# Performance work log

Measured on AMD Instinct MI355X. Metric: run time of the kernel, lower is better.

The kernel has to match this reference:

```python
import jax, jax.numpy as jnp
import numpy as np

STRIDE, PAD, DIL, GROUPS, DG = 1, 1, 1, 1, 1
KH = KW = 3


def setup_inputs() -> dict:
    key = jax.random.key(0)
    k1, k2, k3, k4 = jax.random.split(key, 4)
    N, Cin, Cout, H, W = 8, 256, 256, 64, 64
    Ho = (H + 2 * PAD - (DIL * (KH - 1) + 1)) // STRIDE + 1
    Wo = (W + 2 * PAD - (DIL * (KW - 1) + 1)) // STRIDE + 1
    x = jax.random.normal(k1, (N, Cin, H, W), jnp.float32)
    offset = jax.random.normal(k2, (N, 2 * DG * KH * KW, Ho, Wo), jnp.float32)
    mask = jax.random.uniform(k3, (N, DG * KH * KW, Ho, Wo), jnp.float32)
    fan_in = (Cin // GROUPS) * KH * KW
    weight = jax.random.normal(k4, (Cout, Cin // GROUPS, KH, KW), jnp.float32) * np.float32(np.sqrt(2.0 / fan_in))
    bias = jnp.zeros((Cout,), jnp.float32)
    return {"x": x, "offset": offset, "mask": mask, "weight": weight, "bias": bias}


def _dcn_forward(x, offset, mask, weight, bias):
    # Modulated deformable conv v2 (DCNv2), NCHW layout.
    N, Cin, H, W = x.shape
    Cout, Cg, kh, kw = weight.shape
    K = kh * kw
    Ho, Wo = offset.shape[2], offset.shape[3]
    Cp = Cin // DG  # channels per deformable group

    # offset channels laid out as [DG, K, (dy, dx)]
    off = offset.reshape(N, DG, K, 2, Ho, Wo)
    ky = (jnp.arange(K) // kw) * DIL
    kx = (jnp.arange(K) % kw) * DIL
    base_y = (jnp.arange(Ho) * STRIDE - PAD)[None, :, None] + ky[:, None, None]  # [K,Ho,1]
    base_x = (jnp.arange(Wo) * STRIDE - PAD)[None, None, :] + kx[:, None, None]  # [K,1,Wo]
    y = base_y[None, None] + off[:, :, :, 0]   # [N,DG,K,Ho,Wo] sampling rows
    xs = base_x[None, None] + off[:, :, :, 1]  # [N,DG,K,Ho,Wo] sampling cols

    xg = x.reshape(N, DG, Cp, H * W)  # flat spatial for gathers
    y0 = jnp.floor(y)
    x0 = jnp.floor(xs)
    val = jnp.zeros((N, DG, Cp, K, Ho, Wo), x.dtype)
    # bilinear interpolation with zero padding outside the image
    for iy in (0.0, 1.0):
        for ix in (0.0, 1.0):
            yc = y0 + iy
            xc = x0 + ix
            wgt = (1.0 - jnp.abs(y - yc)) * (1.0 - jnp.abs(xs - xc))
            valid = (yc >= 0) & (yc < H) & (xc >= 0) & (xc < W)
            wgt = jnp.where(valid, wgt, 0.0)
            yci = jnp.clip(yc, 0, H - 1).astype(jnp.int32)
            xci = jnp.clip(xc, 0, W - 1).astype(jnp.int32)
            idx = (yci * W + xci).reshape(N, DG, 1, K * Ho * Wo)
            g = jnp.take_along_axis(xg, idx, axis=3).reshape(N, DG, Cp, K, Ho, Wo)
            val = val + g * wgt[:, :, None]

    # modulation mask, broadcast over channels of each deformable group
    col = val * mask.reshape(N, DG, 1, K, Ho, Wo)
    col = col.reshape(N, GROUPS, Cin // GROUPS, K, Ho, Wo)
    wr = weight.reshape(GROUPS, Cout // GROUPS, Cg, K)
    out = jnp.einsum('gock,ngckhw->ngohw', wr, col).reshape(N, Cout, Ho, Wo)
    return out + bias[None, :, None, None]


def reference(x, offset, mask, weight, bias):
    return _dcn_forward(x, offset, mask, weight, bias)
```

## Files before the change

kernel.cpp:

```cpp
#include <hip/hip_runtime.h>
#include <hip/hip_bf16.h>
#include <stdint.h>


#define XH 64
#define XW 64
#define CIN 256
#define COUT 256
#define NK 9

typedef __attribute__((ext_vector_type(8))) short short8;
typedef __attribute__((ext_vector_type(4))) float floatx4;
typedef __attribute__((ext_vector_type(2))) float floatx2;
typedef __attribute__((ext_vector_type(4))) int   intx4;

__device__ __forceinline__ short f32_to_bf16_rne(float f) {
    union { float f; uint32_t u; } v; v.f = f;
    uint32_t u = v.u;
    uint32_t r = (u + 0x7FFFu + ((u >> 16) & 1u)) >> 16;
    return (short)(uint16_t)r;
}
__device__ __forceinline__ float bf16_to_f32(short s) {
    union { uint32_t u; float f; } v;
    v.u = ((uint32_t)(uint16_t)s) << 16;
    return v.f;
}
__device__ __forceinline__ floatx2 bf16x2_to_f32x2(uint32_t u) {
    union { uint32_t u; float f; } lo, hi;
    lo.u = u << 16;
    hi.u = u & 0xFFFF0000u;
    floatx2 r; r.x = lo.f; r.y = hi.f;
    return r;
}

__global__ void dcn_prep(const float* __restrict__ x, const float* __restrict__ w,
                         short* __restrict__ xT, short* __restrict__ w3) {
    int b = blockIdx.x;
    int tid = threadIdx.x;
    if (b < 512) {
        int xcd = b & 7, slot = b >> 3;
        int h = xcd * 8 + (slot & 7);
        int n = slot >> 3;
        int q = tid & 15;
        int cgh = tid >> 4;
        short8* ob = (short8*)(xT + ((size_t)(n * XH + h)) * (XW * CIN));
        for (int it = 0; it < 2; ++it) {
            int cg = cgh + it * 16;
            const float* xb = x + ((size_t)(n * CIN + cg * 8)) * (XH * XW)
                                + h * XW + q * 4;
            floatx4 r[8];
#pragma unroll
            for (int j = 0; j < 8; ++j)
                r[j] = *(const floatx4*)(xb + (size_t)j * (XH * XW));
#pragma unroll
            for (int jw = 0; jw < 4; ++jw) {
                short8 pk;
#pragma unroll
                for (int j = 0; j < 8; ++j) pk[j] = f32_to_bf16_rne(r[j][jw]);
                ob[(q * 4 + jw) * 32 + cg] = pk;
            }
        }
    } else {
        int gidx = (b - 512) * 256 + tid;
        int lane = gidx & 63;
        int mt   = (gidx >> 6) & 15;
        int t    = gidx >> 10;
        int ks   = t & 7;
        int k    = t >> 3;
        int co = mt * 16 + (lane & 15);
        int c0 = ks * 32 + (lane >> 4) * 8;
        short8 pk;
#pragma unroll
        for (int j = 0; j < 8; ++j)
            pk[j] = f32_to_bf16_rne(w[(co * CIN + c0 + j) * NK + k]);
        *(short8*)&w3[(size_t)gidx * 8] = pk;
    }
}

__launch_bounds__(512, 4)
__global__ void dcn_fused3(const short* __restrict__ xT,
                           const float* __restrict__ off,
                           const float* __restrict__ msk,
                           const short* __restrict__ w3,
                           const float* __restrict__ bias,
                           float* __restrict__ out) {
    __shared__ short   colF[2048 * 8];
    __shared__ floatx4 pairW[576];
    __shared__ intx4   pairO[576];

    const int bid = blockIdx.x;
    const int xcd = bid & 7, slot = bid >> 3;
    const int ho = xcd * 8 + (slot & 7);
    const int n  = slot >> 3;
    const int tid  = threadIdx.x;
    const int wave = tid >> 6;
    const int lane = tid & 63;

    for (int p = tid; p < 576; p += 512) {
        int wo = p & 63, k = p >> 6;
        int obase = ((n * 18 + 2 * k) * XH + ho) * XW + wo;
        float dy = off[obase];
        float dx = off[obase + XH * XW];
        float mm = msk[((n * NK + k) * XH + ho) * XW + wo];
        float y  = (float)(ho - 1 + k / 3) + dy;
        float xs = (float)(wo - 1 + k % 3) + dx;
        float y0f = floorf(y), x0f = floorf(xs);
        float fy = y - y0f, fx = xs - x0f;
        int y0 = (int)y0f, x0 = (int)x0f;
        float vy0 = (y0 >= 0  && y0 < XH)     ? 1.f : 0.f;
        float vy1 = (y0 >= -1 && y0 < XH - 1) ? 1.f : 0.f;
        float vx0 = (x0 >= 0  && x0 < XW)     ? 1.f : 0.f;
        float vx1 = (x0 >= -1 && x0 < XW - 1) ? 1.f : 0.f;
        floatx4 wv;
        wv.x = (1.f - fy) * (1.f - fx) * mm * vy0 * vx0;
        wv.y = (1.f - fy) * fx         * mm * vy0 * vx1;
        wv.z = fy         * (1.f - fx) * mm * vy1 * vx0;
        wv.w = fy         * fx         * mm * vy1 * vx1;
        int y0c = min(max(y0, 0), XH - 1), y1c = min(max(y0 + 1, 0), XH - 1);
        int x0c = min(max(x0, 0), XW - 1), x1c = min(max(x0 + 1, 0), XW - 1);
        intx4 ov;
        ov.x = y0c * XW + x0c; ov.y = y0c * XW + x1c;
        ov.z = y1c * XW + x0c; ov.w = y1c * XW + x1c;
        pairW[p] = wv;
        pairO[p] = ov;
    }
    __syncthreads();

    floatx4 acc[2][4];
#pragma unroll
    for (int mt = 0; mt < 2; ++mt)
#pragma unroll
        for (int nt = 0; nt < 4; ++nt)
            acc[mt][nt] = (floatx4)(0.f);

    const short8* xTv = (const short8*)(xT + (size_t)n * (XH * XW * CIN));
    const short8* w3v = (const short8*)w3;
    const int quad = lane >> 4, cl = lane & 15;

    union U8 { short8 s; uint32_t u[4]; };

    for (int k = 0; k < NK; ++k) {
        if (k) __syncthreads();
        for (int it = 0; it < 4; ++it) {
            int idx = it * 512 + tid;
            int chg = idx & 31;
            int pos = idx >> 5;
            int p = k * 64 + pos;
            floatx4 wv = pairW[p];
            intx4   ov = pairO[p];
            U8 s00, s01, s10, s11, pk;
            s00.s = xTv[(size_t)ov.x * 32 + chg];
            s01.s = xTv[(size_t)ov.y * 32 + chg];
            s10.s = xTv[(size_t)ov.z * 32 + chg];
            s11.s = xTv[(size_t)ov.w * 32 + chg];
#pragma unroll
            for (int i = 0; i < 4; ++i) {
                floatx2 v = bf16x2_to_f32x2(s00.u[i]) * wv.x
                          + bf16x2_to_f32x2(s01.u[i]) * wv.y
                          + bf16x2_to_f32x2(s10.u[i]) * wv.z
                          + bf16x2_to_f32x2(s11.u[i]) * wv.w;
                float2 ff; ff.x = v.x; ff.y = v.y;
                __hip_bfloat162 hb = __float22bfloat162_rn(ff);
                __builtin_memcpy(&pk.u[i], &hb, 4);
            }
            int g = chg * 64 + (pos ^ (chg & 7));
            *(short8*)&colF[g * 8] = pk.s;
        }
        __syncthreads();

        for (int ks = 0; ks < 8; ++ks) {
            short8 afrag[2];
#pragma unroll
            for (int mt = 0; mt < 2; ++mt)
                afrag[mt] = w3v[(((k * 8 + ks) * 16) + (wave * 2 + mt)) * 64 + lane];
            short8 bfrag[4];
            int cr = ks * 4 + quad;
            int gb = cr * 64, sw = cr & 7;
#pragma unroll
            for (int nt = 0; nt < 4; ++nt)
                bfrag[nt] = *(const short8*)&colF[(gb + ((nt * 16 + cl) ^ sw)) * 8];
#pragma unroll
            for (int mt = 0; mt < 2; ++mt)
#pragma unroll
                for (int nt = 0; nt < 4; ++nt)
                    acc[mt][nt] = __builtin_amdgcn_mfma_f32_16x16x32_bf16(
                        afrag[mt], bfrag[nt], acc[mt][nt], 0, 0, 0);
        }
    }

#pragma unroll
    for (int mt = 0; mt < 2; ++mt) {
        int cobase = (wave * 2 + mt) * 16 + quad * 4;
#pragma unroll
        for (int r = 0; r < 4; ++r) {
            int co = cobase + r;
            float b = bias[co];
            float* op = out + (((size_t)n * COUT + co) * XH + ho) * XW;
#pragma unroll
            for (int nt = 0; nt < 4; ++nt)
                op[nt * 16 + cl] = acc[mt][nt][r] + b;
        }
    }
}

__global__ void dcn_wprep_v1(const float* __restrict__ w, short* __restrict__ w3) {
    int idx = blockIdx.x * 256 + threadIdx.x;
    if (idx >= 8 * 9 * 16 * 64 * 8) return;
    int j    = idx & 7;
    int lane = (idx >> 3) & 63;
    int mt   = (idx >> 9) & 15;
    int t    = idx >> 13;
    int ks   = t % 9;
    int cc   = t / 9;
    int co = mt * 16 + (lane & 15);
    int c  = cc * 32 + (lane >> 4) * 8 + j;
    w3[idx] = f32_to_bf16_rne(w[(co * CIN + c) * NK + ks]);
}

__launch_bounds__(256, 2)
__global__ void dcn_fused_v1(const float* __restrict__ x,
                             const float* __restrict__ off,
                             const float* __restrict__ msk,
                             const short* __restrict__ w3,
                             const float* __restrict__ bias,
                             float* __restrict__ out) {
    __shared__ short  colF[2304 * 8];
    __shared__ floatx4 pairW[576];
    __shared__ intx4   pairO[576];

    const int bid = blockIdx.x;
    const int n  = bid >> 6;
    const int ho = bid & 63;
    const int tid  = threadIdx.x;
    const int wave = tid >> 6;
    const int lane = tid & 63;

    for (int p = tid; p < 576; p += 256) {
        int wo = p & 63, k = p >> 6;
        int obase = ((n * 18 + 2 * k) * XH + ho) * XW + wo;
        float dy = off[obase];
        float dx = off[obase + XH * XW];
        float mm = msk[((n * NK + k) * XH + ho) * XW + wo];
        float y  = (float)(ho - 1 + k / 3) + dy;
        float xs = (float)(wo - 1 + k % 3) + dx;
        float y0f = floorf(y), x0f = floorf(xs);
        float fy = y - y0f, fx = xs - x0f;
        int y0 = (int)y0f, x0 = (int)x0f;
        float vy0 = (y0 >= 0  && y0 < XH)     ? 1.f : 0.f;
        float vy1 = (y0 >= -1 && y0 < XH - 1) ? 1.f : 0.f;
        float vx0 = (x0 >= 0  && x0 < XW)     ? 1.f : 0.f;
        float vx1 = (x0 >= -1 && x0 < XW - 1) ? 1.f : 0.f;
        floatx4 wv;
        wv.x = (1.f - fy) * (1.f - fx) * mm * vy0 * vx0;
        wv.y = (1.f - fy) * fx         * mm * vy0 * vx1;
        wv.z = fy         * (1.f - fx) * mm * vy1 * vx0;
        wv.w = fy         * fx         * mm * vy1 * vx1;
        int y0c = min(max(y0, 0), XH - 1), y1c = min(max(y0 + 1, 0), XH - 1);
        int x0c = min(max(x0, 0), XW - 1), x1c = min(max(x0 + 1, 0), XW - 1);
        intx4 ov;
        ov.x = y0c * XW + x0c; ov.y = y0c * XW + x1c;
        ov.z = y1c * XW + x0c; ov.w = y1c * XW + x1c;
        pairW[p] = wv;
        pairO[p] = ov;
    }
    __syncthreads();

    floatx4 acc[4][4];
#pragma unroll
    for (int mt = 0; mt < 4; ++mt)
#pragma unroll
        for (int nt = 0; nt < 4; ++nt)
            acc[mt][nt] = (floatx4)(0.f);

    const float* xn = x + (size_t)n * CIN * (XH * XW);
    const short8* w3v = (const short8*)w3;

    for (int cc = 0; cc < 8; ++cc) {
        __syncthreads();
        for (int it = 0; it < 9; ++it) {
            int item = it * 256 + tid;
            int pos  = item & 63;
            int r    = item >> 6;
            int k    = r >> 2;
            int csub = r & 3;
            int p = k * 64 + pos;
            floatx4 wv = pairW[p];
            intx4   ov = pairO[p];
            const float* xc = xn + (size_t)(cc * 32 + csub * 8) * (XH * XW);
            short8 pk;
#pragma unroll
            for (int i = 0; i < 8; ++i) {
                const float* xp = xc + i * (XH * XW);
                float v = wv.x * xp[ov.x] + wv.y * xp[ov.y] +
                          wv.z * xp[ov.z] + wv.w * xp[ov.w];
                pk[i] = f32_to_bf16_rne(v);
            }
            *(short8*)&colF[(((k * 4 + csub) * 64) + pos) * 8] = pk;
        }
        __syncthreads();

        const int quad = lane >> 4, cl = lane & 15;
        for (int ks = 0; ks < 9; ++ks) {
            short8 afrag[4];
#pragma unroll
            for (int mt = 0; mt < 4; ++mt) {
                int mtg = wave * 4 + mt;
                afrag[mt] = w3v[(((cc * 9 + ks) * 16 + mtg) * 64) + lane];
            }
            short8 bfrag[4];
#pragma unroll
            for (int nt = 0; nt < 4; ++nt)
                bfrag[nt] = *(const short8*)
                    &colF[(((ks * 4 + quad) * 64) + nt * 16 + cl) * 8];
#pragma unroll
            for (int mt = 0; mt < 4; ++mt)
#pragma unroll
                for (int nt = 0; nt < 4; ++nt)
                    acc[mt][nt] = __builtin_amdgcn_mfma_f32_16x16x32_bf16(
                        afrag[mt], bfrag[nt], acc[mt][nt], 0, 0, 0);
        }
    }

    const int quad = lane >> 4, cl = lane & 15;
#pragma unroll
    for (int mt = 0; mt < 4; ++mt) {
        int cobase = (wave * 4 + mt) * 16 + quad * 4;
#pragma unroll
        for (int r = 0; r < 4; ++r) {
            int co = cobase + r;
            float b = bias[co];
            float* op = out + (((size_t)n * COUT + co) * XH + ho) * XW;
#pragma unroll
            for (int nt = 0; nt < 4; ++nt)
                op[nt * 16 + cl] = acc[mt][nt][r] + b;
        }
    }
}

__global__ void dcn_naive(const float* __restrict__ x,
                          const float* __restrict__ off,
                          const float* __restrict__ msk,
                          const float* __restrict__ w,
                          const float* __restrict__ bias,
                          float* __restrict__ out) {
    int idx = blockIdx.x * 256 + threadIdx.x;
    if (idx >= 8 * COUT * XH * XW) return;
    int wo = idx & 63, ho = (idx >> 6) & 63, co = (idx >> 12) & 255, n = idx >> 20;
    float acc = bias[co];
    for (int k = 0; k < NK; ++k) {
        int obase = ((n * 18 + 2 * k) * XH + ho) * XW + wo;
        float dy = off[obase];
        float dx = off[obase + XH * XW];
        float mm = msk[((n * NK + k) * XH + ho) * XW + wo];
        float y  = (float)(ho - 1 + k / 3) + dy;
        float xs = (float)(wo - 1 + k % 3) + dx;
        float y0f = floorf(y), x0f = floorf(xs);
        float fy = y - y0f, fx = xs - x0f;
        int y0 = (int)y0f, x0 = (int)x0f;
        float vy0 = (y0 >= 0  && y0 < XH)     ? 1.f : 0.f;
        float vy1 = (y0 >= -1 && y0 < XH - 1) ? 1.f : 0.f;
        float vx0 = (x0 >= 0  && x0 < XW)     ? 1.f : 0.f;
        float vx1 = (x0 >= -1 && x0 < XW - 1) ? 1.f : 0.f;
        float w00 = (1.f - fy) * (1.f - fx) * mm * vy0 * vx0;
        float w01 = (1.f - fy) * fx         * mm * vy0 * vx1;
        float w10 = fy         * (1.f - fx) * mm * vy1 * vx0;
        float w11 = fy         * fx         * mm * vy1 * vx1;
        int y0c = min(max(y0, 0), XH - 1), y1c = min(max(y0 + 1, 0), XH - 1);
        int x0c = min(max(x0, 0), XW - 1), x1c = min(max(x0 + 1, 0), XW - 1);
        int o00 = y0c * XW + x0c, o01 = y0c * XW + x1c;
        int o10 = y1c * XW + x0c, o11 = y1c * XW + x1c;
        for (int c = 0; c < CIN; ++c) {
            const float* xp = x + ((size_t)(n * CIN + c)) * (XH * XW);
            float v = w00 * xp[o00] + w01 * xp[o01] + w10 * xp[o10] + w11 * xp[o11];
            acc += v * w[(co * CIN + c) * NK + k];
        }
    }
    out[idx] = acc;
}

extern "C" void kernel_launch(void* const* d_in, const int* in_sizes, int n_in,
                              void* d_out, int out_size, void* d_ws, size_t ws_size,
                              hipStream_t stream) {
    const float* x    = (const float*)d_in[0];
    const float* off  = (const float*)d_in[1];
    const float* msk  = (const float*)d_in[2];
    const float* w    = (const float*)d_in[3];
    const float* bias = (const float*)d_in[4];
    float* out = (float*)d_out;

    const size_t W3_BYTES = (size_t)9 * 8 * 16 * 64 * 8 * sizeof(short);
    const size_t XT_BYTES = (size_t)8 * XH * XW * CIN * sizeof(short);

    if (ws_size >= W3_BYTES + XT_BYTES) {
        short* w3 = (short*)d_ws;
        short* xT = (short*)((char*)d_ws + W3_BYTES);
        dcn_prep<<<512 + 288, 256, 0, stream>>>(x, w, xT, w3);
        dcn_fused3<<<8 * 64, 512, 0, stream>>>(xT, off, msk, w3, bias, out);
    } else if (ws_size >= W3_BYTES) {
        short* w3 = (short*)d_ws;
        dcn_wprep_v1<<<(8 * 9 * 16 * 64 * 8 + 255) / 256, 256, 0, stream>>>(w, w3);
        dcn_fused_v1<<<8 * 64, 256, 0, stream>>>(x, off, msk, w3, bias, out);
    } else {
        dcn_naive<<<(8 * COUT * XH * XW + 255) / 256, 256, 0, stream>>>(
            x, off, msk, w, bias, out);
    }
}
```

Baseline: 151.8 us.

## Double-buffer column tile and overlap bilinear gathers with MFMA in half-K steps

The column tile in LDS is split into two half-size buffers, and the reduction is processed in 18 half-channel steps. Each step issues the global gathers for the next step, runs MFMAs on the current buffer, then does the bilinear blend into the other buffer. This needs only one barrier per step instead of two per kernel tap. Gather offsets are also prescaled by 32 to save address math. The cost is more registers held live across the MFMA loop, which at 512 threads with launch bounds of 4 may cause spills or lower occupancy.

```diff
diff --git a/kernel.cpp b/kernel.cpp
--- a/kernel.cpp
+++ b/kernel.cpp
@@ -31,6 +31,25 @@
     hi.u = u & 0xFFFF0000u;
     floatx2 r; r.x = lo.f; r.y = hi.f;
     return r;
+}
+
+union U8 { short8 s; uint32_t u[4]; };
+
+__device__ __forceinline__ short8 bilerp8(const U8& a, const U8& b,
+                                          const U8& c, const U8& d,
+                                          floatx4 wv) {
+    U8 pk;
+#pragma unroll
+    for (int i = 0; i < 4; ++i) {
+        floatx2 v = bf16x2_to_f32x2(a.u[i]) * wv.x
+                  + bf16x2_to_f32x2(b.u[i]) * wv.y
+                  + bf16x2_to_f32x2(c.u[i]) * wv.z
+                  + bf16x2_to_f32x2(d.u[i]) * wv.w;
+        float2 ff; ff.x = v.x; ff.y = v.y;
+        __hip_bfloat162 hb = __float22bfloat162_rn(ff);
+        __builtin_memcpy(&pk.u[i], &hb, 4);
+    }
+    return pk.s;
 }
 
 __global__ void dcn_prep(const float* __restrict__ x, const float* __restrict__ w,
@@ -78,13 +97,13 @@
 }
 
 __launch_bounds__(512, 4)
-__global__ void dcn_fused3(const short* __restrict__ xT,
+__global__ void dcn_fused4(const short* __restrict__ xT,
                            const float* __restrict__ off,
                            const float* __restrict__ msk,
                            const short* __restrict__ w3,
                            const float* __restrict__ bias,
                            float* __restrict__ out) {
-    __shared__ short   colF[2048 * 8];
+    __shared__ short   colF[2][1024 * 8];
     __shared__ floatx4 pairW[576];
     __shared__ intx4   pairO[576];
 
@@ -95,6 +114,7 @@
     const int tid  = threadIdx.x;
     const int wave = tid >> 6;
     const int lane = tid & 63;
+    const int quad = lane >> 4, cl = lane & 15;
 
     for (int p = tid; p < 576; p += 512) {
         int wo = p & 63, k = p >> 6;
@@ -119,8 +139,8 @@
         int y0c = min(max(y0, 0), XH - 1), y1c = min(max(y0 + 1, 0), XH - 1);
         int x0c = min(max(x0, 0), XW - 1), x1c = min(max(x0 + 1, 0), XW - 1);
         intx4 ov;
-        ov.x = y0c * XW + x0c; ov.y = y0c * XW + x1c;
-        ov.z = y1c * XW + x0c; ov.w = y1c * XW + x1c;
+        ov.x = (y0c * XW + x0c) * 32; ov.y = (y0c * XW + x1c) * 32;
+        ov.z = (y1c * XW + x0c) * 32; ov.w = (y1c * XW + x1c) * 32;
         pairW[p] = wv;
         pairO[p] = ov;
     }
@@ -135,57 +155,83 @@
 
     const short8* xTv = (const short8*)(xT + (size_t)n * (XH * XW * CIN));
     const short8* w3v = (const short8*)w3;
-    const int quad = lane >> 4, cl = lane & 15;
-
-    union U8 { short8 s; uint32_t u[4]; };
-
-    for (int k = 0; k < NK; ++k) {
-        if (k) __syncthreads();
-        for (int it = 0; it < 4; ++it) {
+
+    {
+        U8 s[2][4]; floatx4 wv2[2]; int gd[2];
+#pragma unroll
+        for (int it = 0; it < 2; ++it) {
             int idx = it * 512 + tid;
-            int chg = idx & 31;
-            int pos = idx >> 5;
-            int p = k * 64 + pos;
-            floatx4 wv = pairW[p];
-            intx4   ov = pairO[p];
-            U8 s00, s01, s10, s11, pk;
-            s00.s = xTv[(size_t)ov.x * 32 + chg];
-            s01.s = xTv[(size_t)ov.y * 32 + chg];
-            s10.s = xTv[(size_t)ov.z * 32 + chg];
-            s11.s = xTv[(size_t)ov.w * 32 + chg];
-#pragma unroll
-            for (int i = 0; i < 4; ++i) {
-                floatx2 v = bf16x2_to_f32x2(s00.u[i]) * wv.x
-                          + bf16x2_to_f32x2(s01.u[i]) * wv.y
-                          + bf16x2_to_f32x2(s10.u[i]) * wv.z
-                          + bf16x2_to_f32x2(s11.u[i]) * wv.w;
-                float2 ff; ff.x = v.x; ff.y = v.y;
-                __hip_bfloat162 hb = __float22bfloat162_rn(ff);
-                __builtin_memcpy(&pk.u[i], &hb, 4);
+            int chg = idx & 15;
+            int pos = idx >> 4;
+            wv2[it] = pairW[pos];
+            intx4 ov = pairO[pos];
+            s[it][0].s = xTv[ov.x + chg];
+            s[it][1].s = xTv[ov.y + chg];
+            s[it][2].s = xTv[ov.z + chg];
+            s[it][3].s = xTv[ov.w + chg];
+            gd[it] = chg * 64 + (pos ^ (chg & 7));
+        }
+#pragma unroll
+        for (int it = 0; it < 2; ++it)
+            *(short8*)&colF[0][gd[it] * 8] =
+                bilerp8(s[it][0], s[it][1], s[it][2], s[it][3], wv2[it]);
+    }
+    __syncthreads();
+
+    auto step = [&](int ht, const short* rb, short* wb) {
+        const int k = ht >> 1, h = ht & 1;
+        const bool pre = (ht < 17);
+        U8 s[2][4]; floatx4 wv2[2]; int gd[2];
+        if (pre) {
+            const int nht = ht + 1, nk = nht >> 1, nh = nht & 1;
+#pragma unroll
+            for (int it = 0; it < 2; ++it) {
+                int idx = it * 512 + tid;
+                int chg_l = idx & 15;
+                int pos = idx >> 4;
+                int p = nk * 64 + pos;
+                wv2[it] = pairW[p];
+                intx4 ov = pairO[p];
+                int chg = nh * 16 + chg_l;
+                s[it][0].s = xTv[ov.x + chg];
+                s[it][1].s = xTv[ov.y + chg];
+                s[it][2].s = xTv[ov.z + chg];
+                s[it][3].s = xTv[ov.w + chg];
+                gd[it] = chg_l * 64 + (pos ^ (chg_l & 7));
             }
-            int g = chg * 64 + (pos ^ (chg & 7));
-            *(short8*)&colF[g * 8] = pk.s;
-        }
-        __syncthreads();
-
-        for (int ks = 0; ks < 8; ++ks) {
-            short8 afrag[2];
+        }
+        const short8* cb = (const short8*)rb;
+        const int kb = (k * 8 + h * 4) * 16 + wave * 2;
+#pragma unroll
+        for (int ks = 0; ks < 4; ++ks) {
+            const int cr = ks * 4 + quad, sw = cr & 7, gb = cr * 64;
+            short8 afr[2], bfr[4];
 #pragma unroll
             for (int mt = 0; mt < 2; ++mt)
-                afrag[mt] = w3v[(((k * 8 + ks) * 16) + (wave * 2 + mt)) * 64 + lane];
-            short8 bfrag[4];
-            int cr = ks * 4 + quad;
-            int gb = cr * 64, sw = cr & 7;
+                afr[mt] = w3v[(kb + ks * 16 + mt) * 64 + lane];
 #pragma unroll
             for (int nt = 0; nt < 4; ++nt)
-                bfrag[nt] = *(const short8*)&colF[(gb + ((nt * 16 + cl) ^ sw)) * 8];
+                bfr[nt] = cb[gb + ((nt * 16 + cl) ^ sw)];
 #pragma unroll
             for (int mt = 0; mt < 2; ++mt)
 #pragma unroll
                 for (int nt = 0; nt < 4; ++nt)
                     acc[mt][nt] = __builtin_amdgcn_mfma_f32_16x16x32_bf16(
-                        afrag[mt], bfrag[nt], acc[mt][nt], 0, 0, 0);
-        }
+                        afr[mt], bfr[nt], acc[mt][nt], 0, 0, 0);
+        }
+        if (pre) {
+#pragma unroll
+            for (int it = 0; it < 2; ++it)
+                *(short8*)&wb[gd[it] * 8] =
+                    bilerp8(s[it][0], s[it][1], s[it][2], s[it][3], wv2[it]);
+            __syncthreads();
+        }
+    };
+
+#pragma unroll 1
+    for (int hp = 0; hp < 9; ++hp) {
+        step(2 * hp,     colF[0], colF[1]);
+        step(2 * hp + 1, colF[1], colF[0]);
     }
 
 #pragma unroll
@@ -395,7 +441,7 @@
         short* w3 = (short*)d_ws;
         short* xT = (short*)((char*)d_ws + W3_BYTES);
         dcn_prep<<<512 + 288, 256, 0, stream>>>(x, w, xT, w3);
-        dcn_fused3<<<8 * 64, 512, 0, stream>>>(xT, off, msk, w3, bias, out);
+        dcn_fused4<<<8 * 64, 512, 0, stream>>>(xT, off, msk, w3, bias, out);
     } else if (ws_size >= W3_BYTES) {
         short* w3 = (short*)d_ws;
         dcn_wprep_v1<<<(8 * 9 * 16 * 64 * 8 + 255) / 256, 256, 0, stream>>>(w, w3);
```

Measured after the change: 182.2 us. 20.0% more time.

## Double-buffer sampled column tile to overlap gather with MFMA

Applied to the files above, without the earlier changes.

The per-tap column buffer in shared memory is now double-buffered. Bilinear sampling for tap k+1 is written into the spare buffer while the MFMAs for tap k run, which removes one barrier per tap and lets gather latency overlap with matrix math. Pair offsets are also packed as ushort4 to cut their LDS footprint. LDS use per block grows by 32 KB, which may limit how many blocks fit on a CU, and register pressure may rise.

```diff
diff --git a/kernel.cpp b/kernel.cpp
--- a/kernel.cpp
+++ b/kernel.cpp
@@ -32,6 +32,8 @@
     floatx2 r; r.x = lo.f; r.y = hi.f;
     return r;
 }
+
+union U8 { short8 s; uint32_t u[4]; };
 
 __global__ void dcn_prep(const float* __restrict__ x, const float* __restrict__ w,
                          short* __restrict__ xT, short* __restrict__ w3) {
@@ -78,15 +80,15 @@
 }
 
 __launch_bounds__(512, 4)
-__global__ void dcn_fused3(const short* __restrict__ xT,
+__global__ void dcn_fused5(const short* __restrict__ xT,
                            const float* __restrict__ off,
                            const float* __restrict__ msk,
                            const short* __restrict__ w3,
                            const float* __restrict__ bias,
                            float* __restrict__ out) {
-    __shared__ short   colF[2048 * 8];
+    __shared__ short   colF[2][2048 * 8];
     __shared__ floatx4 pairW[576];
-    __shared__ intx4   pairO[576];
+    __shared__ ushort4 pairO[576];
 
     const int bid = blockIdx.x;
     const int xcd = bid & 7, slot = bid >> 3;
@@ -95,6 +97,7 @@
     const int tid  = threadIdx.x;
     const int wave = tid >> 6;
     const int lane = tid & 63;
+    const int quad = lane >> 4, cl = lane & 15;
 
     for (int p = tid; p < 576; p += 512) {
         int wo = p & 63, k = p >> 6;
@@ -118,9 +121,11 @@
         wv.w = fy         * fx         * mm * vy1 * vx1;
         int y0c = min(max(y0, 0), XH - 1), y1c = min(max(y0 + 1, 0), XH - 1);
         int x0c = min(max(x0, 0), XW - 1), x1c = min(max(x0 + 1, 0), XW - 1);
-        intx4 ov;
-        ov.x = y0c * XW + x0c; ov.y = y0c * XW + x1c;
-        ov.z = y1c * XW + x0c; ov.w = y1c * XW + x1c;
+        ushort4 ov;
+        ov.x = (unsigned short)(y0c * XW + x0c);
+        ov.y = (unsigned short)(y0c * XW + x1c);
+        ov.z = (unsigned short)(y1c * XW + x0c);
+        ov.w = (unsigned short)(y1c * XW + x1c);
         pairW[p] = wv;
         pairO[p] = ov;
     }
@@ -135,24 +140,20 @@
 
     const short8* xTv = (const short8*)(xT + (size_t)n * (XH * XW * CIN));
     const short8* w3v = (const short8*)w3;
-    const int quad = lane >> 4, cl = lane & 15;
-
-    union U8 { short8 s; uint32_t u[4]; };
-
-    for (int k = 0; k < NK; ++k) {
-        if (k) __syncthreads();
+
+    auto sampleTap = [&](int k, short* dst) {
         for (int it = 0; it < 4; ++it) {
             int idx = it * 512 + tid;
             int chg = idx & 31;
             int pos = idx >> 5;
             int p = k * 64 + pos;
             floatx4 wv = pairW[p];
-            intx4   ov = pairO[p];
+            ushort4 ov = pairO[p];
             U8 s00, s01, s10, s11, pk;
-            s00.s = xTv[(size_t)ov.x * 32 + chg];
-            s01.s = xTv[(size_t)ov.y * 32 + chg];
-            s10.s = xTv[(size_t)ov.z * 32 + chg];
-            s11.s = xTv[(size_t)ov.w * 32 + chg];
+            s00.s = xTv[(size_t)((int)ov.x * 32) + chg];
+            s01.s = xTv[(size_t)((int)ov.y * 32) + chg];
+            s10.s = xTv[(size_t)((int)ov.z * 32) + chg];
+            s11.s = xTv[(size_t)((int)ov.w * 32) + chg];
 #pragma unroll
             for (int i = 0; i < 4; ++i) {
                 floatx2 v = bf16x2_to_f32x2(s00.u[i]) * wv.x
@@ -164,10 +165,20 @@
                 __builtin_memcpy(&pk.u[i], &hb, 4);
             }
             int g = chg * 64 + (pos ^ (chg & 7));
-            *(short8*)&colF[g * 8] = pk.s;
-        }
-        __syncthreads();
-
+            *(short8*)&dst[g * 8] = pk.s;
+        }
+    };
+
+    sampleTap(0, colF[0]);
+    __syncthreads();
+
+    short* cur = colF[0];
+    short* nxt = colF[1];
+#pragma unroll 1
+    for (int k = 0; k < NK; ++k) {
+        if (k < NK - 1) sampleTap(k + 1, nxt);
+
+        const short8* cb = (const short8*)cur;
         for (int ks = 0; ks < 8; ++ks) {
             short8 afrag[2];
 #pragma unroll
@@ -178,7 +189,7 @@
             int gb = cr * 64, sw = cr & 7;
 #pragma unroll
             for (int nt = 0; nt < 4; ++nt)
-                bfrag[nt] = *(const short8*)&colF[(gb + ((nt * 16 + cl) ^ sw)) * 8];
+                bfrag[nt] = cb[gb + ((nt * 16 + cl) ^ sw)];
 #pragma unroll
             for (int mt = 0; mt < 2; ++mt)
 #pragma unroll
@@ -186,6 +197,9 @@
                     acc[mt][nt] = __builtin_amdgcn_mfma_f32_16x16x32_bf16(
                         afrag[mt], bfrag[nt], acc[mt][nt], 0, 0, 0);
         }
+
+        if (k < NK - 1) __syncthreads();
+        short* t = cur; cur = nxt; nxt = t;
     }
 
 #pragma unroll
@@ -395,7 +409,7 @@
         short* w3 = (short*)d_ws;
         short* xT = (short*)((char*)d_ws + W3_BYTES);
         dcn_prep<<<512 + 288, 256, 0, stream>>>(x, w, xT, w3);
-        dcn_fused3<<<8 * 64, 512, 0, stream>>>(xT, off, msk, w3, bias, out);
+        dcn_fused5<<<8 * 64, 512, 0, stream>>>(xT, off, msk, w3, bias, out);
     } else if (ws_size >= W3_BYTES) {
         short* w3 = (short*)d_ws;
         dcn_wprep_v1<<<(8 * 9 * 16 * 64 * 8 + 255) / 256, 256, 0, stream>>>(w, w3);
```

New measurement: 161.3 us. 1.06x slower.
